# Kernel optimization log

Hardware: AMD Instinct MI355X
Metric: run time of the kernel (lower is better)

Reference implementation:

```python
import jax, jax.numpy as jnp
import numpy as np

N, L, K = 2048, 256, 16

def setup_inputs() -> dict:
    rng = np.random.default_rng(0)
    # per level: wavelet index = l (distinct across levels), plus K-1 random distinct rest indices
    sel = np.zeros((L, K), dtype=np.int64)
    wav = np.arange(L, dtype=np.int64)
    all_idx = np.arange(N)
    for l in range(L):
        others = rng.choice(np.delete(all_idx, l), size=K - 1, replace=False)
        sel[l] = np.sort(np.concatenate([[l], others]))
    key = jax.random.key(0)
    k1, k2 = jax.random.split(key)
    M = jax.random.normal(k1, (N, N), dtype=jnp.float32)
    A = 0.5 * (M + M.T)  # symmetric matrix, as MMF expects
    O_all = jax.random.normal(k2, (L, K, K), dtype=jnp.float32) / np.float32(K) ** 0.5
    return {"A": A, "O_all": O_all, "sel_idx": jnp.asarray(sel), "wav_idx": jnp.asarray(wav)}


def reference(A, O_all, sel_idx, wav_idx):
    # Torch builds a dense NxN U = eye with O scattered into the KxK block at
    # sel_idx x sel_idx, then A <- U A U^T and right <- U @ right.
    # Equivalent efficient form: only the K selected rows/cols change.
    n = A.shape[0]

    def step(carry, xs):
        A, right = carry
        O, idx = xs  # O: (K,K), idx: (K,)
        A = A.at[idx].set(O @ A[idx])              # U @ A   : rewrite K rows
        A = A.at[:, idx].set(A[:, idx] @ O.T)      # ... @ U^T: rewrite K cols
        right = right.at[idx].set(O @ right[idx])  # right <- U @ right
        return (A, right), None

    right0 = jnp.eye(n, dtype=A.dtype)
    (A_f, right), _ = jax.lax.scan(step, (A, right0), (O_all, sel_idx))

    # final_active_index: 1 everywhere except wavelet indices
    active = jnp.ones((n,), dtype=A.dtype).at[wav_idx].set(0.0)
    # left_index = eye - diag(diag(outer)) + outer  -> diag all ones, off-diag = a_i*a_j
    left = jnp.outer(active, active)
    left = left.at[jnp.diag_indices(n)].set(1.0)
    D = A_f * left
    A_rec = right.T @ D @ right
    return (A_rec, right, D)
```

## Files before the change

kernel.cpp:

```cpp
#include <hip/hip_runtime.h>

#define N 2048
#define LEV 256
#define KS 16

typedef __attribute__((ext_vector_type(8))) short bfx8;
typedef __attribute__((ext_vector_type(4))) float fx4;
typedef unsigned short u16;
typedef unsigned int u32;

static const size_t NN = (size_t)N * N;

__device__ inline u16 bf16_rne(float f) {
    u32 u = __builtin_bit_cast(u32, f);
    u32 r = (u + 0x7FFFu + ((u >> 16) & 1u)) >> 16;
    return (u16)r;
}
__device__ inline float bf16_f(u16 h) {
    u32 u = ((u32)h) << 16;
    return __builtin_bit_cast(float, u);
}

#define GLDS16(gp, lp) __builtin_amdgcn_global_load_lds( \
    (const __attribute__((address_space(1))) void*)(uintptr_t)(gp), \
    (__attribute__((address_space(3))) void*)(u32)(uintptr_t)(lp), 16, 0, 0)

__device__ inline float qadd(float x) {
#if __has_builtin(__builtin_amdgcn_mov_dpp)
    int a = __builtin_amdgcn_mov_dpp(__builtin_bit_cast(int, x), 0xB1, 0xF, 0xF, true);
    float y = x + __builtin_bit_cast(float, a);
    int b = __builtin_amdgcn_mov_dpp(__builtin_bit_cast(int, y), 0x4E, 0xF, 0xF, true);
    return y + __builtin_bit_cast(float, b);
#else
    float y = x + __shfl_xor(x, 1);
    return y + __shfl_xor(y, 2);
#endif
}

__global__ __launch_bounds__(64)
void front_k(const float* __restrict__ O_all, const int* __restrict__ sel,
             float* __restrict__ RT, u16* __restrict__ rth,
             const float* __restrict__ A, u16* __restrict__ a2h) {
    __shared__ float x[2048];
    const int lane = threadIdx.x;

    if (blockIdx.x >= 2048) {
        u16* a2l = a2h + NN;
        size_t p = (((size_t)blockIdx.x - 2048) * 64 + lane) * 8;
        float4 v0 = *(const float4*)(A + p);
        float4 v1 = *(const float4*)(A + p + 4);
        float vv[8] = {v0.x, v0.y, v0.z, v0.w, v1.x, v1.y, v1.z, v1.w};
        bfx8 hs, ls;
        #pragma unroll
        for (int i = 0; i < 8; ++i) {
            u16 h = bf16_rne(vv[i]);
            hs[i] = (short)h;
            ls[i] = (short)bf16_rne(vv[i] - bf16_f(h));
        }
        *(bfx8*)(a2h + p) = hs;
        *(bfx8*)(a2l + p) = ls;
        return;
    }

    const int i    = lane >> 2;
    const int kg   = lane & 3;
    const int col  = blockIdx.x;

    const float4 z = make_float4(0.f, 0.f, 0.f, 0.f);
    #pragma unroll
    for (int q = 0; q < 8; ++q) *(float4*)&x[q * 256 + lane * 4] = z;
    if (lane == 0) x[col] = 1.0f;

    const float* obase = O_all + i * KS + kg * 4;
    const int*   gbase = sel + kg * 4;

#define CMP(f, g, wv) { \
    float p = f.x * x[g.x] + f.y * x[g.y] + f.z * x[g.z] + f.w * x[g.w]; \
    p = qadd(p); \
    if (kg == 0) x[wv] = p; }

    float4 f0 = *(const float4*)(obase);
    int4   g0 = *(const int4*)(gbase);
    int    w0 = sel[i];
    float4 f1 = *(const float4*)(obase + 256);
    int4   g1 = *(const int4*)(gbase + KS);
    int    w1 = sel[KS + i];

    for (int l = 0; l < LEV; l += 2) {
        float4 f2, f3; int4 g2, g3; int w2, w3;
        if (l + 2 < LEV) {
            f2 = *(const float4*)(obase + (size_t)(l + 2) * 256);
            g2 = *(const int4*)(gbase + (l + 2) * KS);
            w2 = sel[(l + 2) * KS + i];
            f3 = *(const float4*)(obase + (size_t)(l + 3) * 256);
            g3 = *(const int4*)(gbase + (l + 3) * KS);
            w3 = sel[(l + 3) * KS + i];
        } else { f2 = f0; g2 = g0; w2 = w0; f3 = f1; g3 = g1; w3 = w1; }

        CMP(f0, g0, w0)
        CMP(f1, g1, w1)
        f0 = f2; g0 = g2; w0 = w2;
        f1 = f3; g1 = g3; w1 = w3;
    }
#undef CMP

    u16* rtl = rth + NN;
    #pragma unroll
    for (int q = 0; q < 8; ++q) {
        float4 v = *(const float4*)&x[q * 256 + lane * 4];
        *(float4*)&RT[(size_t)col * N + q * 256 + lane * 4] = v;
        float vv[4] = {v.x, v.y, v.z, v.w};
        u16 hh[4], ll[4];
        #pragma unroll
        for (int e = 0; e < 4; ++e) {
            hh[e] = bf16_rne(vv[e]);
            ll[e] = bf16_rne(vv[e] - bf16_f(hh[e]));
        }
        const size_t po = (size_t)col * N + q * 256 + lane * 4;
        *(ushort4*)(rth + po) = make_ushort4(hh[0], hh[1], hh[2], hh[3]);
        *(ushort4*)(rtl + po) = make_ushort4(ll[0], ll[1], ll[2], ll[3]);
    }
}

__global__ __launch_bounds__(256)
void split_rt_k(const float* __restrict__ RT, u16* __restrict__ r2h,
                float* __restrict__ Rrm) {
    __shared__ float t[64][65];
    u16* r2l = r2h + NN;
    const int r0 = (blockIdx.x >> 5) * 64, c0 = (blockIdx.x & 31) * 64;
    #pragma unroll
    for (int i = 0; i < 16; ++i) {
        int q = i * 256 + threadIdx.x;
        int rr = q >> 6, cc = q & 63;
        t[rr][cc] = RT[(size_t)(r0 + rr) * N + c0 + cc];
    }
    __syncthreads();
    #pragma unroll
    for (int i = 0; i < 16; ++i) {
        int q = i * 256 + threadIdx.x;
        int rr = q >> 6, cc = q & 63;
        float w = t[cc][rr];
        u16 h2 = bf16_rne(w);
        size_t pt = (size_t)(c0 + rr) * N + r0 + cc;
        r2h[pt] = h2;
        r2l[pt] = bf16_rne(w - bf16_f(h2));
        Rrm[pt] = w;
    }
}

__global__ __launch_bounds__(256)
void unsplit_k(const u16* __restrict__ hi, float* __restrict__ dst) {
    const u16* lo = hi + NN;
    size_t p = ((size_t)blockIdx.x * 256 + threadIdx.x) * 8;
    bfx8 hs = *(const bfx8*)(hi + p);
    bfx8 ls = *(const bfx8*)(lo + p);
    float4 o0, o1;
    o0.x = bf16_f((u16)hs[0]) + bf16_f((u16)ls[0]);
    o0.y = bf16_f((u16)hs[1]) + bf16_f((u16)ls[1]);
    o0.z = bf16_f((u16)hs[2]) + bf16_f((u16)ls[2]);
    o0.w = bf16_f((u16)hs[3]) + bf16_f((u16)ls[3]);
    o1.x = bf16_f((u16)hs[4]) + bf16_f((u16)ls[4]);
    o1.y = bf16_f((u16)hs[5]) + bf16_f((u16)ls[5]);
    o1.z = bf16_f((u16)hs[6]) + bf16_f((u16)ls[6]);
    o1.w = bf16_f((u16)hs[7]) + bf16_f((u16)ls[7]);
    *(float4*)(dst + p)     = o0;
    *(float4*)(dst + p + 4) = o1;
}

template<int MASKED, int OMODE>
__global__ __launch_bounds__(256)
void gemm_bf3(const u16* __restrict__ Xp, const u16* __restrict__ Yp,
              float* __restrict__ Cf, u16* __restrict__ Cs,
              const int* __restrict__ wav, int Lw) {
    __shared__ __align__(16) u16 sm[24576];
    __shared__ float rowf[128], colf[64];

    const int tid = threadIdx.x;
    const int xcd = blockIdx.x & 7, idx = blockIdx.x >> 3;
    const int sup = 4 * xcd + (idx >> 4);
    const int wi4 = idx & 15;
    const int by = (sup >> 3) * 4 + (wi4 >> 2);
    const int bx = (sup & 7) * 4 + (wi4 & 3);
    const int i0 = by * 128, j0 = bx * 64;
    const int lane = tid & 63, w = tid >> 6;
    const int wm = (w >> 1) * 64, wn = (w & 1) * 32;
    const int fr = lane & 15;

    if (MASKED) {
        if (tid < 128) rowf[tid] = 1.0f;
        if (tid >= 128 && tid < 192) colf[tid - 128] = 1.0f;
        __syncthreads();
        for (int t = tid; t < Lw; t += 256) {
            int wv = wav[t];
            int dr = wv - i0; if (0 <= dr && dr < 128) rowf[dr] = 0.0f;
            int dc = wv - j0; if (0 <= dc && dc < 64)  colf[dc] = 0.0f;
        }
    }

    fx4 acc[4][2];
    #pragma unroll
    for (int m = 0; m < 4; ++m)
        #pragma unroll
        for (int n = 0; n < 2; ++n)
            acc[m][n] = (fx4)0.0f;

    const u16* Xh = Xp; const u16* Xl = Xp + NN;
    const u16* Yh = Yp; const u16* Yl = Yp + NN;

    const int rl   = lane >> 3;
    const int gcol = ((lane & 7) ^ rl) << 3;
    const int wq   = w * 1024;

    #define STAGE(kt) { \
        const int k0s = (kt) * 64; \
        char* lb0 = (char*)sm + wq; \
        _Pragma("unroll") \
        for (int q = 0; q < 4; ++q) { \
            const int row = q * 32 + w * 8 + rl; \
            const size_t xo = (size_t)(i0 + row) * N + k0s + gcol; \
            GLDS16(Xh + xo, lb0 + q * 4096); \
            GLDS16(Xl + xo, lb0 + 16384 + q * 4096); \
        } \
        _Pragma("unroll") \
        for (int q = 0; q < 2; ++q) { \
            const int row = q * 32 + w * 8 + rl; \
            const size_t yo = (size_t)(j0 + row) * N + k0s + gcol; \
            GLDS16(Yh + yo, lb0 + 32768 + q * 4096); \
            GLDS16(Yl + yo, lb0 + 40960 + q * 4096); \
        } }

    const int kq  = (lane >> 4) << 4;
    const int frx = (fr & 7) << 4;

    #define COMPUTE() { \
        const char* base = (const char*)sm; \
        _Pragma("unroll") \
        for (int s = 0; s < 2; ++s) { \
            const int cb = s * 64 + kq; \
            bfx8 ah[4], al[4]; \
            _Pragma("unroll") \
            for (int m = 0; m < 4; ++m) { \
                const int off = (wm + m * 16 + fr) * 128 + (cb ^ frx); \
                ah[m] = *(const bfx8*)(base + off); \
                al[m] = *(const bfx8*)(base + 16384 + off); \
            } \
            _Pragma("unroll") \
            for (int n = 0; n < 2; ++n) { \
                const int off = (wn + n * 16 + fr) * 128 + (cb ^ frx); \
                bfx8 bh = *(const bfx8*)(base + 32768 + off); \
                bfx8 bl = *(const bfx8*)(base + 40960 + off); \
                _Pragma("unroll") \
                for (int m = 0; m < 4; ++m) { \
                    acc[m][n] = __builtin_amdgcn_mfma_f32_16x16x32_bf16(ah[m], bh, acc[m][n], 0, 0, 0); \
                    acc[m][n] = __builtin_amdgcn_mfma_f32_16x16x32_bf16(ah[m], bl, acc[m][n], 0, 0, 0); \
                    acc[m][n] = __builtin_amdgcn_mfma_f32_16x16x32_bf16(al[m], bh, acc[m][n], 0, 0, 0); \
                } \
            } \
        } }

    constexpr int NT = N / 64;
    for (int kt = 0; kt < NT; ++kt) {
        STAGE(kt)
        __syncthreads();
        COMPUTE()
        __syncthreads();
    }

    const int crow0 = (lane >> 4) * 4;
    #pragma unroll
    for (int m = 0; m < 4; ++m) {
        #pragma unroll
        for (int n = 0; n < 2; ++n) {
            #pragma unroll
            for (int r = 0; r < 4; ++r) {
                const int li = wm + m * 16 + crow0 + r;
                const int lj = wn + n * 16 + fr;
                float v = acc[m][n][r];
                if (MASKED) {
                    if (i0 + li != j0 + lj) v *= rowf[li] * colf[lj];
                }
                const size_t off = (size_t)(i0 + li) * N + j0 + lj;
                if (OMODE == 0) {
                    Cf[off] = v;
                } else {
                    u16 h = bf16_rne(v);
                    Cs[off]      = h;
                    Cs[NN + off] = bf16_rne(v - bf16_f(h));
                }
            }
        }
    }
    #undef STAGE
    #undef COMPUTE
}

template<int MASKED, int OMODE>
__global__ __launch_bounds__(256)
void gemm_sym(const u16* __restrict__ Xp, const u16* __restrict__ Yp,
              float* __restrict__ Cf, u16* __restrict__ Cs,
              const int* __restrict__ wav, int Lw) {
    __shared__ __align__(16) u16 sm[16384];
    __shared__ float rowf[64], colf[64];

    const int tid = threadIdx.x;
    int swz = (blockIdx.x & 7) * 66 + (blockIdx.x >> 3);
    int t = swz, by = 0;
    #pragma unroll 1
    while (t >= 32 - by) { t -= 32 - by; ++by; }
    const int bx = by + t;
    const int i0 = by * 64, j0 = bx * 64;
    const int lane = tid & 63, w = tid >> 6;
    const int wm = (w >> 1) * 32, wn = (w & 1) * 32;
    const int fr = lane & 15;

    if (MASKED) {
        if (tid < 64) rowf[tid] = 1.0f;
        if (tid >= 128 && tid < 192) colf[tid - 128] = 1.0f;
        __syncthreads();
        for (int t2 = tid; t2 < Lw; t2 += 256) {
            int wv = wav[t2];
            int dr = wv - i0; if (0 <= dr && dr < 64) rowf[dr] = 0.0f;
            int dc = wv - j0; if (0 <= dc && dc < 64) colf[dc] = 0.0f;
        }
    }

    fx4 acc[2][2];
    #pragma unroll
    for (int m = 0; m < 2; ++m)
        #pragma unroll
        for (int n = 0; n < 2; ++n)
            acc[m][n] = (fx4)0.0f;

    const u16* Xh = Xp; const u16* Xl = Xp + NN;
    const u16* Yh = Yp; const u16* Yl = Yp + NN;

    const int rl   = lane >> 3;
    const int gcol = ((lane & 7) ^ rl) << 3;
    const int wq   = w * 1024;
    const int kq   = (lane >> 4) << 4;
    const int frx  = (fr & 7) << 4;

    constexpr int NT = N / 64;
    for (int kt = 0; kt < NT; ++kt) {
        const int k0s = kt * 64;
        {
            char* lb0 = (char*)sm + wq;
            #pragma unroll
            for (int q = 0; q < 2; ++q) {
                const int row = q * 32 + w * 8 + rl;
                const size_t xo = (size_t)(i0 + row) * N + k0s + gcol;
                const size_t yo = (size_t)(j0 + row) * N + k0s + gcol;
                GLDS16(Xh + xo, lb0 + q * 4096);
                GLDS16(Xl + xo, lb0 + 8192 + q * 4096);
                GLDS16(Yh + yo, lb0 + 16384 + q * 4096);
                GLDS16(Yl + yo, lb0 + 24576 + q * 4096);
            }
        }
        __syncthreads();
        {
            const char* base = (const char*)sm;
            #pragma unroll
            for (int s = 0; s < 2; ++s) {
                const int cb = s * 64 + kq;
                bfx8 ah[2], al[2];
                #pragma unroll
                for (int m = 0; m < 2; ++m) {
                    const int off = (wm + m * 16 + fr) * 128 + (cb ^ frx);
                    ah[m] = *(const bfx8*)(base + off);
                    al[m] = *(const bfx8*)(base + 8192 + off);
                }
                #pragma unroll
                for (int n = 0; n < 2; ++n) {
                    const int off = (wn + n * 16 + fr) * 128 + (cb ^ frx);
                    bfx8 bh = *(const bfx8*)(base + 16384 + off);
                    bfx8 bl = *(const bfx8*)(base + 24576 + off);
                    #pragma unroll
                    for (int m = 0; m < 2; ++m) {
                        acc[m][n] = __builtin_amdgcn_mfma_f32_16x16x32_bf16(ah[m], bh, acc[m][n], 0, 0, 0);
                        acc[m][n] = __builtin_amdgcn_mfma_f32_16x16x32_bf16(ah[m], bl, acc[m][n], 0, 0, 0);
                        acc[m][n] = __builtin_amdgcn_mfma_f32_16x16x32_bf16(al[m], bh, acc[m][n], 0, 0, 0);
                    }
                }
            }
        }
        __syncthreads();
    }

    float* Ct = (float*)sm;
    const int crow0 = (lane >> 4) * 4;
    #pragma unroll
    for (int m = 0; m < 2; ++m) {
        #pragma unroll
        for (int n = 0; n < 2; ++n) {
            #pragma unroll
            for (int r = 0; r < 4; ++r) {
                const int li = wm + m * 16 + crow0 + r;
                const int lj = wn + n * 16 + fr;
                float v = acc[m][n][r];
                if (MASKED) {
                    if (i0 + li != j0 + lj) v *= rowf[li] * colf[lj];
                }
                Ct[li * 65 + lj] = v;
                const size_t off = (size_t)(i0 + li) * N + j0 + lj;
                if (OMODE == 0) {
                    Cf[off] = v;
                } else {
                    u16 h = bf16_rne(v);
                    Cs[off]      = h;
                    Cs[NN + off] = bf16_rne(v - bf16_f(h));
                }
            }
        }
    }

    if (by != bx) {
        __syncthreads();
        const int rr  = tid >> 2;
        const int cc0 = (tid & 3) * 16;
        float v[16];
        #pragma unroll
        for (int e = 0; e < 16; ++e) v[e] = Ct[(cc0 + e) * 65 + rr];
        const size_t off = (size_t)(j0 + rr) * N + i0 + cc0;
        if (OMODE == 0) {
            #pragma unroll
            for (int q = 0; q < 4; ++q)
                *(float4*)(Cf + off + q * 4) =
                    make_float4(v[q*4], v[q*4+1], v[q*4+2], v[q*4+3]);
        } else {
            bfx8 hs[2], ls[2];
            #pragma unroll
            for (int e = 0; e < 16; ++e) {
                u16 h = bf16_rne(v[e]);
                hs[e >> 3][e & 7] = (short)h;
                ls[e >> 3][e & 7] = (short)bf16_rne(v[e] - bf16_f(h));
            }
            *(bfx8*)(Cs + off)          = hs[0];
            *(bfx8*)(Cs + off + 8)      = hs[1];
            *(bfx8*)(Cs + NN + off)     = ls[0];
            *(bfx8*)(Cs + NN + off + 8) = ls[1];
        }
    }
}

extern "C" void kernel_launch(void* const* d_in, const int* in_sizes, int n_in,
                              void* d_out, int out_size, void* d_ws, size_t ws_size,
                              hipStream_t stream) {
    const float* A     = (const float*)d_in[0];
    const float* O_all = (const float*)d_in[1];
    const int*   sel   = (const int*)d_in[2];
    const int*   wav   = (const int*)d_in[3];
    const int    Lw    = in_sizes[3];

    float* O1 = (float*)d_out;
    float* O2 = O1 + NN;
    float* O3 = O1 + 2 * NN;

    u16*   W1u = (u16*)d_ws;
    u16*   W2u = (u16*)((char*)d_ws + 2 * NN * sizeof(u16));
    u16*   O1u = (u16*)O1;
    u16*   O3u = (u16*)O3;

    const int SGRID = (int)(NN / (256 * 8));

    front_k<<<2048 + (int)(NN / (64 * 8)), 64, 0, stream>>>(O_all, sel, O3, W1u, A, W2u);
    split_rt_k<<<(N / 64) * (N / 64), 256, 0, stream>>>(O3, O1u, O2);

    gemm_bf3<0, 1><<<512, 256, 0, stream>>>(O1u, W2u, nullptr, O3u, nullptr, 0);
    gemm_sym<1, 1><<<528, 256, 0, stream>>>(O3u, O1u, nullptr, W2u, wav, Lw);
    gemm_bf3<0, 1><<<512, 256, 0, stream>>>(W1u, W2u, nullptr, O3u, nullptr, 0);
    gemm_sym<0, 0><<<528, 256, 0, stream>>>(O3u, W1u, O1, nullptr, nullptr, 0);
    unsplit_k<<<SGRID, 256, 0, stream>>>(W2u, O3);
}
```

Before: 243.5 us.

## Prefetch next level's LDS gathers speculatively, using overlap flags to refetch on conflict

Adds a tiny kernel that flags each level whose selected indices overlap the previous level's. The sequential 256-level rotation loop in front_k now issues the LDS reads for level l+1 before level l's reduction and store. It reuses those early values unless the flag shows a dependency, in which case it rereads them. This is meant to take LDS read latency off the serial dependency chain, at the cost of one extra kernel launch and a flags buffer stored in the output region.

Measured after the change: 278.0 us. +14.2%, slower.

```diff
diff --git a/kernel.cpp b/kernel.cpp
--- a/kernel.cpp
+++ b/kernel.cpp
@@ -37,8 +37,26 @@
 #endif
 }
 
+__global__ __launch_bounds__(256)
+void flags_k(const int* __restrict__ sel, int* __restrict__ flags) {
+    const int l = threadIdx.x;
+    int f = 0;
+    if (l > 0) {
+        int a[KS], b[KS];
+        #pragma unroll
+        for (int k = 0; k < KS; ++k) { a[k] = sel[l * KS + k]; b[k] = sel[(l - 1) * KS + k]; }
+        #pragma unroll
+        for (int i = 0; i < KS; ++i)
+            #pragma unroll
+            for (int j = 0; j < KS; ++j)
+                f |= (a[i] == b[j]);
+    }
+    flags[l] = f;
+}
+
 __global__ __launch_bounds__(64)
 void front_k(const float* __restrict__ O_all, const int* __restrict__ sel,
+             const int* __restrict__ flags,
              float* __restrict__ RT, u16* __restrict__ rth,
              const float* __restrict__ A, u16* __restrict__ a2h) {
     __shared__ float x[2048];
@@ -74,35 +92,43 @@
     const float* obase = O_all + i * KS + kg * 4;
     const int*   gbase = sel + kg * 4;
 
-#define CMP(f, g, wv) { \
-    float p = f.x * x[g.x] + f.y * x[g.y] + f.z * x[g.z] + f.w * x[g.w]; \
-    p = qadd(p); \
-    if (kg == 0) x[wv] = p; }
-
-    float4 f0 = *(const float4*)(obase);
-    int4   g0 = *(const int4*)(gbase);
-    int    w0 = sel[i];
-    float4 f1 = *(const float4*)(obase + 256);
-    int4   g1 = *(const int4*)(gbase + KS);
-    int    w1 = sel[KS + i];
-
-    for (int l = 0; l < LEV; l += 2) {
-        float4 f2, f3; int4 g2, g3; int w2, w3;
+    float4 o_c = *(const float4*)(obase);
+    int4   g_c = *(const int4*)(gbase);
+    int    w_c = sel[i];
+    int    fl_c = 0;
+    float4 o_n = *(const float4*)(obase + 256);
+    int4   g_n = *(const int4*)(gbase + KS);
+    int    w_n = sel[KS + i];
+    int    fl_n = flags[1];
+
+    float gv0 = x[g_c.x], gv1 = x[g_c.y], gv2 = x[g_c.z], gv3 = x[g_c.w];
+
+    for (int l = 0; l < LEV; ++l) {
+        float4 o_p; int4 g_p; int w_p, fl_p;
         if (l + 2 < LEV) {
-            f2 = *(const float4*)(obase + (size_t)(l + 2) * 256);
-            g2 = *(const int4*)(gbase + (l + 2) * KS);
-            w2 = sel[(l + 2) * KS + i];
-            f3 = *(const float4*)(obase + (size_t)(l + 3) * 256);
-            g3 = *(const int4*)(gbase + (l + 3) * KS);
-            w3 = sel[(l + 3) * KS + i];
-        } else { f2 = f0; g2 = g0; w2 = w0; f3 = f1; g3 = g1; w3 = w1; }
-
-        CMP(f0, g0, w0)
-        CMP(f1, g1, w1)
-        f0 = f2; g0 = g2; w0 = w2;
-        f1 = f3; g1 = g3; w1 = w3;
-    }
-#undef CMP
+            o_p  = *(const float4*)(obase + (size_t)(l + 2) * 256);
+            g_p  = *(const int4*)(gbase + (l + 2) * KS);
+            w_p  = sel[(l + 2) * KS + i];
+            fl_p = flags[l + 2];
+        } else { o_p = o_n; g_p = g_n; w_p = w_n; fl_p = 0; }
+
+        float v0, v1, v2, v3;
+        if (fl_c) {
+            v0 = x[g_c.x]; v1 = x[g_c.y]; v2 = x[g_c.z]; v3 = x[g_c.w];
+        } else {
+            v0 = gv0; v1 = gv1; v2 = gv2; v3 = gv3;
+        }
+
+        float n0 = x[g_n.x], n1 = x[g_n.y], n2 = x[g_n.z], n3 = x[g_n.w];
+
+        float p = o_c.x * v0 + o_c.y * v1 + o_c.z * v2 + o_c.w * v3;
+        p = qadd(p);
+        if (kg == 0) x[w_c] = p;
+
+        gv0 = n0; gv1 = n1; gv2 = n2; gv3 = n3;
+        o_c = o_n; g_c = g_n; w_c = w_n; fl_c = fl_n;
+        o_n = o_p; g_n = g_p; w_n = w_p; fl_n = fl_p;
+    }
 
     u16* rtl = rth + NN;
     #pragma unroll
@@ -459,10 +485,12 @@
     u16*   W2u = (u16*)((char*)d_ws + 2 * NN * sizeof(u16));
     u16*   O1u = (u16*)O1;
     u16*   O3u = (u16*)O3;
+    int*   flg = (int*)O1;
 
     const int SGRID = (int)(NN / (256 * 8));
 
-    front_k<<<2048 + (int)(NN / (64 * 8)), 64, 0, stream>>>(O_all, sel, O3, W1u, A, W2u);
+    flags_k<<<1, 256, 0, stream>>>(sel, flg);
+    front_k<<<2048 + (int)(NN / (64 * 8)), 64, 0, stream>>>(O_all, sel, flg, O3, W1u, A, W2u);
     split_rt_k<<<(N / 64) * (N / 64), 256, 0, stream>>>(O3, O1u, O2);
 
     gemm_bf3<0, 1><<<512, 256, 0, stream>>>(O1u, W2u, nullptr, O3u, nullptr, 0);
```
